# Kernel optimization log

Hardware: AMD Instinct MI355X
Metric: run time of the kernel (lower is better)

Reference implementation:

```python
import jax, jax.numpy as jnp
import numpy as np

B, L, D, H = 8, 512, 512, 8
E, G = 4, 2            # primary experts, ghost experts
THRESH = 0.01          # ghost_activation_threshold
EPS = 1e-5             # LayerNorm eps (torch default)


def _ln(x, s, b):
    m = x.mean(-1, keepdims=True)
    v = ((x - m) ** 2).mean(-1, keepdims=True)
    return (x - m) * jax.lax.rsqrt(v + EPS) * s + b


def _expert(x, ln1_s, ln1_b, wqkv, bqkv, wo, bo, ln2_s, ln2_b, w1, b1, w2, b2):
    # Pre-norm transformer block: MHA + residual, FFN + residual (dropout=0)
    Bn, Ln, Dn = x.shape
    dh = Dn // H
    xn = _ln(x, ln1_s, ln1_b)
    qkv = xn @ wqkv + bqkv                      # [B,L,3D]
    q, k, v = jnp.split(qkv, 3, axis=-1)
    heads = lambda t: t.reshape(Bn, Ln, H, dh).transpose(0, 2, 1, 3)
    q, k, v = heads(q), heads(k), heads(v)      # [B,H,L,dh]
    scores = jnp.einsum('bhqd,bhkd->bhqk', q, k) / np.sqrt(dh).astype(np.float32)
    attn = jax.nn.softmax(scores, axis=-1)
    o = jnp.einsum('bhqk,bhkd->bhqd', attn, v).transpose(0, 2, 1, 3).reshape(Bn, Ln, Dn)
    x = x + o @ wo + bo
    h = _ln(x, ln2_s, ln2_b)
    x = x + jax.nn.gelu(h @ w1 + b1) @ w2 + b2
    return x


def _make_params(key, n, d):
    ks = jax.random.split(key, 4)
    s = 0.02
    return dict(
        ln1_s=jnp.ones((n, d)), ln1_b=jnp.zeros((n, d)),
        wqkv=jax.random.normal(ks[0], (n, d, 3 * d)) * s, bqkv=jnp.zeros((n, 3 * d)),
        wo=jax.random.normal(ks[1], (n, d, d)) * s, bo=jnp.zeros((n, d)),
        ln2_s=jnp.ones((n, d)), ln2_b=jnp.zeros((n, d)),
        w1=jax.random.normal(ks[2], (n, d, 4 * d)) * s, b1=jnp.zeros((n, 4 * d)),
        w2=jax.random.normal(ks[3], (n, 4 * d, d)) * s, b2=jnp.zeros((n, d)))


def setup_inputs() -> dict:
    key = jax.random.key(0)
    k1, k2, k3 = jax.random.split(key, 3)
    inp = {'x': jax.random.normal(k1, (B, L, D), jnp.float32), 'step': 100}
    for pre, n, k in (('p_', E, k2), ('g_', G, k3)):
        for name, arr in _make_params(k, n, D).items():
            inp[pre + name] = arr
    return inp


def reference(x, step,
              p_ln1_s, p_ln1_b, p_wqkv, p_bqkv, p_wo, p_bo, p_ln2_s, p_ln2_b, p_w1, p_b1, p_w2, p_b2,
              g_ln1_s, g_ln1_b, g_wqkv, g_bqkv, g_wo, g_bo, g_ln2_s, g_ln2_b, g_w1, g_b1, g_w2, g_b2):
    pp = (p_ln1_s, p_ln1_b, p_wqkv, p_bqkv, p_wo, p_bo, p_ln2_s, p_ln2_b, p_w1, p_b1, p_w2, p_b2)
    gp = (g_ln1_s, g_ln1_b, g_wqkv, g_bqkv, g_wo, g_bo, g_ln2_s, g_ln2_b, g_w1, g_b1, g_w2, g_b2)
    run = jax.vmap(lambda ps: _expert(x, *ps))
    prim = run(pp)                               # [E,B,L,D]
    # --- saturation metrics (statistics only; detached like .item() in torch) ---
    mean_eo = prim.mean(axis=(1, 2))             # [E,D]
    nrm = mean_eo / jnp.linalg.norm(mean_eo, axis=1, keepdims=True)
    gram = nrm @ nrm.T                           # [E,E]
    ortho = 1.0 - jnp.mean((gram - jnp.eye(E, dtype=gram.dtype)) ** 2)
    recon = prim.mean(axis=0)                    # [B,L,D]
    uvar = jnp.var(x - recon, ddof=1)            # torch.var unbiased default
    sat = jax.lax.stop_gradient(ortho * uvar)
    # --- ghost activation (initial state: all dormant -> ghost 0 gets 0.01) ---
    base = jnp.zeros((G,), x.dtype).at[0].set(0.01)
    rates = jnp.where(sat > THRESH, base, jnp.zeros((G,), x.dtype))
    ghost = jax.vmap(lambda ps: _expert(x, *ps))(gp) * rates[:, None, None, None]  # [G,B,L,D]
    # combine: mean over all (primary + ghost) expert outputs
    out = jnp.concatenate([prim, ghost], axis=0).mean(axis=0)  # [B,L,D]
    return out
```

## Files before the change

### kernel.cpp

```cpp
#include <hip/hip_runtime.h>

typedef __bf16 bf16;
typedef __bf16 bf16x8 __attribute__((ext_vector_type(8)));
typedef float  f32x4  __attribute__((ext_vector_type(4)));

#define AS1 __attribute__((address_space(1)))
#define AS3 __attribute__((address_space(3)))

__device__ __forceinline__ void async16(const void* g, void* l) {
  __builtin_amdgcn_global_load_lds((const AS1 unsigned int*)g, (AS3 unsigned int*)l, 16, 0, 0);
}

__device__ __forceinline__ float gelu_tanh(float u) {
  return 0.5f * u * (1.f + tanhf(0.7978845608028654f * (u + 0.044715f * u * u * u)));
}

__global__ __launch_bounds__(256) void transpose_cvt(const float* pbase, const float* gbase,
                                                     bf16* dst, int K, int M) {
  __shared__ float tile[32][33];
  const int z = blockIdx.z;
  const float* src = (z < 4) ? pbase + (size_t)z * K * M : gbase;
  bf16* d = dst + (size_t)z * M * K;
  const int mBlk = blockIdx.x * 32, kBlk = blockIdx.y * 32;
  for (int i = 0; i < 4; i++)
    tile[threadIdx.y + i * 8][threadIdx.x] =
        src[(size_t)(kBlk + threadIdx.y + i * 8) * M + mBlk + threadIdx.x];
  __syncthreads();
  for (int i = 0; i < 4; i++)
    d[(size_t)(mBlk + threadIdx.y + i * 8) * K + kBlk + threadIdx.x] =
        (bf16)tile[threadIdx.x][threadIdx.y + i * 8];
}

__global__ __launch_bounds__(256) void ln_kernel(const float* in, long long inStrideZ,
                                                 const float* sP, const float* bP,
                                                 const float* sG, const float* bG, bf16* out) {
  const int t = blockIdx.x, z = blockIdx.y, tid = threadIdx.x;
  const float* xr = in + (size_t)z * inStrideZ + (size_t)t * 512;
  float v0 = xr[tid], v1 = xr[tid + 256];
  float s1 = v0 + v1, s2 = v0 * v0 + v1 * v1;
  for (int off = 32; off > 0; off >>= 1) { s1 += __shfl_down(s1, off); s2 += __shfl_down(s2, off); }
  __shared__ float red[8];
  __shared__ float mv[2];
  const int wv = tid >> 6, ln = tid & 63;
  if (ln == 0) { red[wv] = s1; red[4 + wv] = s2; }
  __syncthreads();
  if (tid == 0) {
    float a = red[0] + red[1] + red[2] + red[3];
    float b = red[4] + red[5] + red[6] + red[7];
    float mean = a * (1.f / 512.f);
    float var = b * (1.f / 512.f) - mean * mean;
    mv[0] = mean; mv[1] = 1.f / sqrtf(var + 1e-5f);
  }
  __syncthreads();
  const float mean = mv[0], rs = mv[1];
  const float* sc = (z < 4) ? sP + (size_t)z * 512 : sG;
  const float* bi = (z < 4) ? bP + (size_t)z * 512 : bG;
  bf16* orow = out + (size_t)z * 4096 * 512 + (size_t)t * 512;
  orow[tid]       = (bf16)((v0 - mean) * rs * sc[tid] + bi[tid]);
  orow[tid + 256] = (bf16)((v1 - mean) * rs * sc[tid + 256] + bi[tid + 256]);
}

template <int MODE>
__global__ __launch_bounds__(256, 2) void gemm_bt(
    const bf16* Abase, const bf16* Wt, const float* biasP, const float* biasG,
    int K, int M, void* out, const float* resid, long long residStrideZ,
    float* prim_sum, float* mean_acc, float* ghost_out) {
  const int bx = blockIdx.x, by = blockIdx.y, z = blockIdx.z;
  const bf16* A = Abase + (size_t)z * 4096 * K;
  const bf16* B = Wt + (size_t)z * M * K;
  const float* bias = (z < 4) ? biasP + (size_t)z * M : biasG;
  __shared__ bf16 As[128 * 64];
  __shared__ bf16 Bs[128 * 64];
  const int tid = threadIdx.x, wave = tid >> 6, l = tid & 63;
  const int m16 = l & 15, q4 = l >> 4;
  const int wm = wave & 1, wn = wave >> 1;
  f32x4 zero4 = {0.f, 0.f, 0.f, 0.f};
  f32x4 acc[4][4];
  for (int i = 0; i < 4; i++) for (int j = 0; j < 4; j++) acc[i][j] = zero4;
  const int rowA0 = by * 128, rowB0 = bx * 128;

  for (int kt = 0; kt < K; kt += 64) {
    __syncthreads();
    for (int i = 0; i < 4; i++) {
      int s = i * 256 + tid, r = s >> 3, kb = s & 7;
      int col = kt + ((kb ^ (r & 7)) << 3);
      async16(A + (size_t)(rowA0 + r) * K + col, &As[(i * 256 + wave * 64) * 8]);
      async16(B + (size_t)(rowB0 + r) * K + col, &Bs[(i * 256 + wave * 64) * 8]);
    }
    __syncthreads();
    for (int ks = 0; ks < 2; ks++) {
      bf16x8 af[4], bfr[4];
      for (int mi = 0; mi < 4; mi++) {
        int r = wm * 64 + mi * 16 + m16, kb = ks * 4 + q4;
        af[mi] = *(const bf16x8*)&As[r * 64 + ((kb ^ (r & 7)) << 3)];
      }
      for (int ni = 0; ni < 4; ni++) {
        int r = wn * 64 + ni * 16 + m16, kb = ks * 4 + q4;
        bfr[ni] = *(const bf16x8*)&Bs[r * 64 + ((kb ^ (r & 7)) << 3)];
      }
      for (int mi = 0; mi < 4; mi++)
        for (int ni = 0; ni < 4; ni++)
          acc[mi][ni] = __builtin_amdgcn_mfma_f32_16x16x32_bf16(af[mi], bfr[ni], acc[mi][ni], 0, 0, 0);
    }
  }

  const int col0 = rowB0 + wn * 64, row0 = rowA0 + wm * 64;
  if constexpr (MODE == 3) {
    for (int ni = 0; ni < 4; ni++) {
      int col = col0 + ni * 16 + m16;
      float bb = bias[col];
      float csum = 0.f;
      for (int mi = 0; mi < 4; mi++) {
        for (int cr = 0; cr < 4; cr++) {
          int row = row0 + mi * 16 + q4 * 4 + cr;
          float v = acc[mi][ni][cr] + bb +
                    resid[(size_t)z * residStrideZ + (size_t)row * 512 + col];
          if (z < 4) { atomicAdd(&prim_sum[(size_t)row * 512 + col], v); csum += v; }
          else ghost_out[(size_t)row * 512 + col] = v;
        }
      }
      if (z < 4) {
        csum += __shfl_xor(csum, 16);
        csum += __shfl_xor(csum, 32);
        if (q4 == 0) atomicAdd(&mean_acc[z * 512 + col], csum);
      }
    }
  } else {
    for (int ni = 0; ni < 4; ni++) {
      int col = col0 + ni * 16 + m16;
      float bb = bias[col];
      for (int mi = 0; mi < 4; mi++) {
        for (int cr = 0; cr < 4; cr++) {
          int row = row0 + mi * 16 + q4 * 4 + cr;
          float v = acc[mi][ni][cr] + bb;
          if constexpr (MODE == 0) {
            ((bf16*)out)[(size_t)z * 4096 * M + (size_t)row * M + col] = (bf16)v;
          } else if constexpr (MODE == 1) {
            v += resid[(size_t)row * 512 + col];
            ((float*)out)[(size_t)z * 4096 * 512 + (size_t)row * 512 + col] = v;
          } else {
            ((bf16*)out)[(size_t)z * 4096 * M + (size_t)row * M + col] = (bf16)gelu_tanh(v);
          }
        }
      }
    }
  }
}

__global__ __launch_bounds__(256, 2) void attn_kernel(const bf16* qkv, bf16* o) {
  const int qt = blockIdx.x, bh = blockIdx.y, z = blockIdx.z;
  const int b = bh >> 3, h = bh & 7;
  const bf16* base = qkv + (size_t)z * 4096 * 1536 + (size_t)b * 512 * 1536;
  __shared__ bf16 Qs[128 * 64];
  __shared__ bf16 Ks[64 * 64];
  __shared__ bf16 Vt[64 * 72];
  __shared__ bf16 Ps[4][32 * 72];
  const int tid = threadIdx.x, wave = tid >> 6, l = tid & 63;
  const int m16 = l & 15, q4 = l >> 4;
  f32x4 zero4 = {0.f, 0.f, 0.f, 0.f};

  for (int i = 0; i < 4; i++) {
    int s = i * 256 + tid, r = s >> 3, kb = s & 7;
    async16(base + (size_t)(qt * 128 + r) * 1536 + h * 64 + ((kb ^ (r & 7)) << 3),
            &Qs[(i * 256 + wave * 64) * 8]);
  }
  f32x4 Oacc[2][4];
  float m_run[2][4], l_run[2][4];
  for (int rt = 0; rt < 2; rt++)
    for (int cr = 0; cr < 4; cr++) { m_run[rt][cr] = -3.0e38f; l_run[rt][cr] = 0.f; }
  for (int rt = 0; rt < 2; rt++) for (int dt = 0; dt < 4; dt++) Oacc[rt][dt] = zero4;
  __syncthreads();
  bf16x8 qf[2][2];
  for (int rt = 0; rt < 2; rt++)
    for (int ks = 0; ks < 2; ks++) {
      int r = wave * 32 + rt * 16 + m16, kb = ks * 4 + q4;
      qf[rt][ks] = *(const bf16x8*)&Qs[r * 64 + ((kb ^ (r & 7)) << 3)];
    }

  for (int kt = 0; kt < 8; kt++) {
    __syncthreads();
    for (int i = 0; i < 2; i++) {
      int s = i * 256 + tid, r = s >> 3, kb = s & 7;
      async16(base + (size_t)(kt * 64 + r) * 1536 + 512 + h * 64 + ((kb ^ (r & 7)) << 3),
              &Ks[(i * 256 + wave * 64) * 8]);
    }
    {
      int d = tid & 63, kbase = (tid >> 6) * 2;
      for (int i = 0; i < 8; i++) {
        int k0 = kbase + i * 8;
        bf16 a0 = base[(size_t)(kt * 64 + k0) * 1536 + 1024 + h * 64 + d];
        bf16 a1 = base[(size_t)(kt * 64 + k0 + 1) * 1536 + 1024 + h * 64 + d];
        Vt[d * 72 + k0] = a0; Vt[d * 72 + k0 + 1] = a1;
      }
    }
    __syncthreads();
    f32x4 S[2][4];
    for (int rt = 0; rt < 2; rt++)
      for (int ct = 0; ct < 4; ct++) {
        f32x4 a = zero4;
        for (int ks = 0; ks < 2; ks++) {
          int n = ct * 16 + m16, kb = ks * 4 + q4;
          bf16x8 kf = *(const bf16x8*)&Ks[n * 64 + ((kb ^ (n & 7)) << 3)];
          a = __builtin_amdgcn_mfma_f32_16x16x32_bf16(qf[rt][ks], kf, a, 0, 0, 0);
        }
        S[rt][ct] = a * 0.125f;
      }
    float alpha[2][4];
    for (int rt = 0; rt < 2; rt++)
      for (int cr = 0; cr < 4; cr++) {
        float mx = fmaxf(fmaxf(S[rt][0][cr], S[rt][1][cr]), fmaxf(S[rt][2][cr], S[rt][3][cr]));
        mx = fmaxf(mx, __shfl_xor(mx, 1)); mx = fmaxf(mx, __shfl_xor(mx, 2));
        mx = fmaxf(mx, __shfl_xor(mx, 4)); mx = fmaxf(mx, __shfl_xor(mx, 8));
        float mnew = fmaxf(m_run[rt][cr], mx);
        float al = __expf(m_run[rt][cr] - mnew);
        m_run[rt][cr] = mnew;
        float rs = 0.f;
        for (int ct = 0; ct < 4; ct++) {
          float p = __expf(S[rt][ct][cr] - mnew);
          S[rt][ct][cr] = p; rs += p;
        }
        rs += __shfl_xor(rs, 1); rs += __shfl_xor(rs, 2);
        rs += __shfl_xor(rs, 4); rs += __shfl_xor(rs, 8);
        l_run[rt][cr] = l_run[rt][cr] * al + rs;
        alpha[rt][cr] = al;
      }
    for (int rt = 0; rt < 2; rt++)
      for (int dt = 0; dt < 4; dt++)
        for (int cr = 0; cr < 4; cr++) Oacc[rt][dt][cr] *= alpha[rt][cr];
    bf16* pw = &Ps[wave][0];
    for (int rt = 0; rt < 2; rt++)
      for (int ct = 0; ct < 4; ct++)
        for (int cr = 0; cr < 4; cr++)
          pw[(rt * 16 + q4 * 4 + cr) * 72 + ct * 16 + m16] = (bf16)S[rt][ct][cr];
    for (int rt = 0; rt < 2; rt++)
      for (int dt = 0; dt < 4; dt++) {
        f32x4 a = Oacc[rt][dt];
        for (int ks = 0; ks < 2; ks++) {
          bf16x8 pf = *(const bf16x8*)&pw[(rt * 16 + m16) * 72 + ks * 32 + q4 * 8];
          bf16x8 vf = *(const bf16x8*)&Vt[(dt * 16 + m16) * 72 + ks * 32 + q4 * 8];
          a = __builtin_amdgcn_mfma_f32_16x16x32_bf16(pf, vf, a, 0, 0, 0);
        }
        Oacc[rt][dt] = a;
      }
  }
  bf16* ob = o + (size_t)z * 4096 * 512 + (size_t)(b * 512 + qt * 128 + wave * 32) * 512 + h * 64;
  for (int rt = 0; rt < 2; rt++)
    for (int dt = 0; dt < 4; dt++)
      for (int cr = 0; cr < 4; cr++) {
        int r = rt * 16 + q4 * 4 + cr;
        ob[(size_t)r * 512 + dt * 16 + m16] = (bf16)(Oacc[rt][dt][cr] / l_run[rt][cr]);
      }
}

__global__ __launch_bounds__(256) void stats_diff(const float* x, const float* ps, float* accum) {
  const int tid0 = blockIdx.x * blockDim.x + threadIdx.x;
  float s = 0.f, s2 = 0.f;
  const f32x4* xv = (const f32x4*)x;
  const f32x4* pv = (const f32x4*)ps;
  for (int it = 0; it < 2; it++) {
    int i = tid0 + it * 262144;
    f32x4 d = xv[i] - pv[i] * 0.25f;
    s += d[0] + d[1] + d[2] + d[3];
    s2 += d[0] * d[0] + d[1] * d[1] + d[2] * d[2] + d[3] * d[3];
  }
  for (int off = 32; off > 0; off >>= 1) { s += __shfl_down(s, off); s2 += __shfl_down(s2, off); }
  __shared__ float r1[4], r2[4];
  if ((threadIdx.x & 63) == 0) { r1[threadIdx.x >> 6] = s; r2[threadIdx.x >> 6] = s2; }
  __syncthreads();
  if (threadIdx.x == 0) {
    atomicAdd(&accum[0], r1[0] + r1[1] + r1[2] + r1[3]);
    atomicAdd(&accum[1], r2[0] + r2[1] + r2[2] + r2[3]);
  }
}

__global__ void finalize_k(const float* mean_acc, const float* accum, float* rate) {
  const int l = threadIdx.x;
  float me[4][8];
  for (int e = 0; e < 4; e++)
    for (int j = 0; j < 8; j++) me[e][j] = mean_acc[e * 512 + l * 8 + j] * (1.f / 4096.f);
  float dot[4][4];
  for (int e = 0; e < 4; e++)
    for (int f = e; f < 4; f++) {
      float d = 0.f;
      for (int j = 0; j < 8; j++) d += me[e][j] * me[f][j];
      for (int off = 32; off > 0; off >>= 1) d += __shfl_xor(d, off);
      dot[e][f] = d; dot[f][e] = d;
    }
  float nrm[4];
  for (int e = 0; e < 4; e++) nrm[e] = sqrtf(dot[e][e]);
  float acc = 0.f;
  for (int e = 0; e < 4; e++)
    for (int f = 0; f < 4; f++) {
      float g = dot[e][f] / (nrm[e] * nrm[f]) - (e == f ? 1.f : 0.f);
      acc += g * g;
    }
  float ortho = 1.f - acc * (1.f / 16.f);
  float n = 2097152.f;
  float uvar = (accum[1] - accum[0] * accum[0] / n) / (n - 1.f);
  float sat = ortho * uvar;
  if (l == 0) rate[0] = (sat > 0.01f) ? 0.01f : 0.f;
}

__global__ __launch_bounds__(256) void combine_k(const float* prim, const float* ghost,
                                                 const float* rate, float* out) {
  float r = rate[0];
  int i = blockIdx.x * blockDim.x + threadIdx.x;
  const f32x4* p = (const f32x4*)prim;
  const f32x4* g = (const f32x4*)ghost;
  ((f32x4*)out)[i] = (p[i] + r * g[i]) * (1.f / 6.f);
}

extern "C" void kernel_launch(void* const* d_in, const int* in_sizes, int n_in,
                              void* d_out, int out_size, void* d_ws, size_t ws_size,
                              hipStream_t stream) {
  const float* x       = (const float*)d_in[0];
  const float* p_ln1_s = (const float*)d_in[2];
  const float* p_ln1_b = (const float*)d_in[3];
  const float* p_wqkv  = (const float*)d_in[4];
  const float* p_bqkv  = (const float*)d_in[5];
  const float* p_wo    = (const float*)d_in[6];
  const float* p_bo    = (const float*)d_in[7];
  const float* p_ln2_s = (const float*)d_in[8];
  const float* p_ln2_b = (const float*)d_in[9];
  const float* p_w1    = (const float*)d_in[10];
  const float* p_b1    = (const float*)d_in[11];
  const float* p_w2    = (const float*)d_in[12];
  const float* p_b2    = (const float*)d_in[13];
  const float* g_ln1_s = (const float*)d_in[14];
  const float* g_ln1_b = (const float*)d_in[15];
  const float* g_wqkv  = (const float*)d_in[16];
  const float* g_bqkv  = (const float*)d_in[17];
  const float* g_wo    = (const float*)d_in[18];
  const float* g_bo    = (const float*)d_in[19];
  const float* g_ln2_s = (const float*)d_in[20];
  const float* g_ln2_b = (const float*)d_in[21];
  const float* g_w1    = (const float*)d_in[22];
  const float* g_b1    = (const float*)d_in[23];
  const float* g_w2    = (const float*)d_in[24];
  const float* g_b2    = (const float*)d_in[25];

  char* ws = (char*)d_ws;
  size_t off = 0;
  auto alloc = [&](size_t bytes) { void* p = ws + off; off += (bytes + 255) & ~(size_t)255; return p; };
  bf16* wt_qkv   = (bf16*)alloc(5ull * 1536 * 512 * 2);
  bf16* wt_wo    = (bf16*)alloc(5ull * 512 * 512 * 2);
  bf16* wt_w1    = (bf16*)alloc(5ull * 2048 * 512 * 2);
  bf16* wt_w2    = (bf16*)alloc(5ull * 512 * 2048 * 2);
  bf16* act_a    = (bf16*)alloc(5ull * 4096 * 512 * 2);
  bf16* big      = (bf16*)alloc(5ull * 4096 * 2048 * 2);
  float* x1      = (float*)alloc(5ull * 4096 * 512 * 4);
  float* prim_sum  = (float*)alloc(4096ull * 512 * 4);
  float* ghost_out = (float*)alloc(4096ull * 512 * 4);
  float* mean_acc  = (float*)alloc(4 * 512 * 4);
  float* accum     = (float*)alloc(256);

  hipMemsetAsync(prim_sum, 0, 4096ull * 512 * 4, stream);
  hipMemsetAsync(mean_acc, 0, 4 * 512 * 4, stream);
  hipMemsetAsync(accum, 0, 16, stream);

  dim3 tb(32, 8);
  transpose_cvt<<<dim3(1536 / 32, 512 / 32, 5), tb, 0, stream>>>(p_wqkv, g_wqkv, wt_qkv, 512, 1536);
  transpose_cvt<<<dim3(512 / 32, 512 / 32, 5), tb, 0, stream>>>(p_wo, g_wo, wt_wo, 512, 512);
  transpose_cvt<<<dim3(2048 / 32, 512 / 32, 5), tb, 0, stream>>>(p_w1, g_w1, wt_w1, 512, 2048);
  transpose_cvt<<<dim3(512 / 32, 2048 / 32, 5), tb, 0, stream>>>(p_w2, g_w2, wt_w2, 2048, 512);

  ln_kernel<<<dim3(4096, 5), 256, 0, stream>>>(x, 0, p_ln1_s, p_ln1_b, g_ln1_s, g_ln1_b, act_a);
  gemm_bt<0><<<dim3(12, 32, 5), 256, 0, stream>>>(act_a, wt_qkv, p_bqkv, g_bqkv, 512, 1536,
                                                  big, nullptr, 0, nullptr, nullptr, nullptr);
  attn_kernel<<<dim3(4, 64, 5), 256, 0, stream>>>(big, act_a);
  gemm_bt<1><<<dim3(4, 32, 5), 256, 0, stream>>>(act_a, wt_wo, p_bo, g_bo, 512, 512,
                                                 x1, x, 0, nullptr, nullptr, nullptr);
  ln_kernel<<<dim3(4096, 5), 256, 0, stream>>>(x1, 4096ll * 512, p_ln2_s, p_ln2_b, g_ln2_s, g_ln2_b, act_a);
  gemm_bt<2><<<dim3(16, 32, 5), 256, 0, stream>>>(act_a, wt_w1, p_b1, g_b1, 512, 2048,
                                                  big, nullptr, 0, nullptr, nullptr, nullptr);
  gemm_bt<3><<<dim3(4, 32, 5), 256, 0, stream>>>(big, wt_w2, p_b2, g_b2, 2048, 512,
                                                 nullptr, x1, 4096ll * 512, prim_sum, mean_acc, ghost_out);
  stats_diff<<<dim3(1024), 256, 0, stream>>>(x, prim_sum, accum);
  finalize_k<<<1, 64, 0, stream>>>(mean_acc, accum, accum + 2);
  combine_k<<<dim3(2048), 256, 0, stream>>>(prim_sum, ghost_out, accum + 2, (float*)d_out);
}
```

Baseline: 546.7 us.

## Fold LN1 into QKV weights, store bf16 intermediates, stage GEMM epilogues via LDS

```diff
diff --git a/kernel.cpp b/kernel.cpp
--- a/kernel.cpp
+++ b/kernel.cpp
@@ -11,38 +11,57 @@
   __builtin_amdgcn_global_load_lds((const AS1 unsigned int*)g, (AS3 unsigned int*)l, 16, 0, 0);
 }
 
-__device__ __forceinline__ float gelu_tanh(float u) {
-  return 0.5f * u * (1.f + tanhf(0.7978845608028654f * (u + 0.044715f * u * u * u)));
-}
-
-__global__ __launch_bounds__(256) void transpose_cvt(const float* pbase, const float* gbase,
-                                                     bf16* dst, int K, int M) {
+__device__ __forceinline__ float gelu_fast(float u) {
+  float z = 0.7978845608028654f * (u + 0.044715f * u * u * u);
+  z = fminf(fmaxf(z, -15.f), 15.f);
+  float t = __expf(2.f * z);
+  return u * t / (t + 1.f);
+}
+
+template <int FOLD>
+__global__ __launch_bounds__(256) void transpose_cvt(
+    const float* pbase, const float* gbase, bf16* dst, int K, int M,
+    const float* lnsP, const float* lnbP, const float* lnsG, const float* lnbG,
+    const float* b0P, const float* b0G, float* bias_eff) {
   __shared__ float tile[32][33];
   const int z = blockIdx.z;
   const float* src = (z < 4) ? pbase + (size_t)z * K * M : gbase;
   bf16* d = dst + (size_t)z * M * K;
   const int mBlk = blockIdx.x * 32, kBlk = blockIdx.y * 32;
+  const int tx = threadIdx.x, ty = threadIdx.y;
   for (int i = 0; i < 4; i++)
-    tile[threadIdx.y + i * 8][threadIdx.x] =
-        src[(size_t)(kBlk + threadIdx.y + i * 8) * M + mBlk + threadIdx.x];
-  __syncthreads();
-  for (int i = 0; i < 4; i++)
-    d[(size_t)(mBlk + threadIdx.y + i * 8) * K + kBlk + threadIdx.x] =
-        (bf16)tile[threadIdx.x][threadIdx.y + i * 8];
-}
-
-__global__ __launch_bounds__(256) void ln_kernel(const float* in, long long inStrideZ,
-                                                 const float* sP, const float* bP,
-                                                 const float* sG, const float* bG, bf16* out) {
-  const int t = blockIdx.x, z = blockIdx.y, tid = threadIdx.x;
-  const float* xr = in + (size_t)z * inStrideZ + (size_t)t * 512;
+    tile[ty + i * 8][tx] = src[(size_t)(kBlk + ty + i * 8) * M + mBlk + tx];
+  __syncthreads();
+  if constexpr (FOLD) {
+    const float* s  = (z < 4) ? lnsP + (size_t)z * 512 : lnsG;
+    const float* bb = (z < 4) ? lnbP + (size_t)z * 512 : lnbG;
+    const float sk = s[kBlk + tx];
+    for (int i = 0; i < 4; i++)
+      d[(size_t)(mBlk + ty + i * 8) * K + kBlk + tx] = (bf16)(tile[tx][ty + i * 8] * sk);
+    if (ty == 0) {
+      float acc = 0.f;
+      for (int kk = 0; kk < 32; kk++) acc += bb[kBlk + kk] * tile[kk][tx];
+      if (kBlk == 0) {
+        const float* b0 = (z < 4) ? b0P + (size_t)z * M : b0G;
+        acc += b0[mBlk + tx];
+      }
+      atomicAdd(&bias_eff[(size_t)z * M + mBlk + tx], acc);
+    }
+  } else {
+    for (int i = 0; i < 4; i++)
+      d[(size_t)(mBlk + ty + i * 8) * K + kBlk + tx] = (bf16)tile[tx][ty + i * 8];
+  }
+}
+
+__global__ __launch_bounds__(256) void ln_plain(const float* x, bf16* out) {
+  const int t = blockIdx.x, tid = threadIdx.x;
+  const float* xr = x + (size_t)t * 512;
   float v0 = xr[tid], v1 = xr[tid + 256];
   float s1 = v0 + v1, s2 = v0 * v0 + v1 * v1;
   for (int off = 32; off > 0; off >>= 1) { s1 += __shfl_down(s1, off); s2 += __shfl_down(s2, off); }
   __shared__ float red[8];
   __shared__ float mv[2];
-  const int wv = tid >> 6, ln = tid & 63;
-  if (ln == 0) { red[wv] = s1; red[4 + wv] = s2; }
+  if ((tid & 63) == 0) { red[tid >> 6] = s1; red[4 + (tid >> 6)] = s2; }
   __syncthreads();
   if (tid == 0) {
     float a = red[0] + red[1] + red[2] + red[3];
@@ -53,24 +72,50 @@
   }
   __syncthreads();
   const float mean = mv[0], rs = mv[1];
+  bf16* o = out + (size_t)t * 512;
+  o[tid]       = (bf16)((v0 - mean) * rs);
+  o[tid + 256] = (bf16)((v1 - mean) * rs);
+}
+
+__global__ __launch_bounds__(256) void ln2_kernel(const bf16* in, const float* sP, const float* bP,
+                                                  const float* sG, const float* bG, bf16* out) {
+  const int t = blockIdx.x, z = blockIdx.y, tid = threadIdx.x;
+  const bf16* xr = in + (size_t)z * 4096 * 512 + (size_t)t * 512;
+  float v0 = (float)xr[tid], v1 = (float)xr[tid + 256];
+  float s1 = v0 + v1, s2 = v0 * v0 + v1 * v1;
+  for (int off = 32; off > 0; off >>= 1) { s1 += __shfl_down(s1, off); s2 += __shfl_down(s2, off); }
+  __shared__ float red[8];
+  __shared__ float mv[2];
+  if ((tid & 63) == 0) { red[tid >> 6] = s1; red[4 + (tid >> 6)] = s2; }
+  __syncthreads();
+  if (tid == 0) {
+    float a = red[0] + red[1] + red[2] + red[3];
+    float b = red[4] + red[5] + red[6] + red[7];
+    float mean = a * (1.f / 512.f);
+    float var = b * (1.f / 512.f) - mean * mean;
+    mv[0] = mean; mv[1] = 1.f / sqrtf(var + 1e-5f);
+  }
+  __syncthreads();
+  const float mean = mv[0], rs = mv[1];
   const float* sc = (z < 4) ? sP + (size_t)z * 512 : sG;
   const float* bi = (z < 4) ? bP + (size_t)z * 512 : bG;
-  bf16* orow = out + (size_t)z * 4096 * 512 + (size_t)t * 512;
-  orow[tid]       = (bf16)((v0 - mean) * rs * sc[tid] + bi[tid]);
-  orow[tid + 256] = (bf16)((v1 - mean) * rs * sc[tid + 256] + bi[tid + 256]);
+  bf16* o = out + (size_t)z * 4096 * 512 + (size_t)t * 512;
+  o[tid]       = (bf16)((v0 - mean) * rs * sc[tid] + bi[tid]);
+  o[tid + 256] = (bf16)((v1 - mean) * rs * sc[tid + 256] + bi[tid + 256]);
 }
 
 template <int MODE>
 __global__ __launch_bounds__(256, 2) void gemm_bt(
-    const bf16* Abase, const bf16* Wt, const float* biasP, const float* biasG,
-    int K, int M, void* out, const float* resid, long long residStrideZ,
-    float* prim_sum, float* mean_acc, float* ghost_out) {
+    const bf16* Abase, long long aStrideZ, const bf16* Wt,
+    const float* biasP, const float* biasG, int K, int M,
+    bf16* out, const void* resid, long long residStrideZ) {
   const int bx = blockIdx.x, by = blockIdx.y, z = blockIdx.z;
-  const bf16* A = Abase + (size_t)z * 4096 * K;
+  const bf16* A = Abase + (size_t)z * aStrideZ;
   const bf16* B = Wt + (size_t)z * M * K;
   const float* bias = (z < 4) ? biasP + (size_t)z * M : biasG;
-  __shared__ bf16 As[128 * 64];
-  __shared__ bf16 Bs[128 * 64];
+  __shared__ bf16 smem[128 * 136];
+  bf16* As = smem;
+  bf16* Bs = smem + 128 * 64;
   const int tid = threadIdx.x, wave = tid >> 6, l = tid & 63;
   const int m16 = l & 15, q4 = l >> 4;
   const int wm = wave & 1, wn = wave >> 1;
@@ -104,46 +149,32 @@
     }
   }
 
-  const int col0 = rowB0 + wn * 64, row0 = rowA0 + wm * 64;
-  if constexpr (MODE == 3) {
-    for (int ni = 0; ni < 4; ni++) {
-      int col = col0 + ni * 16 + m16;
-      float bb = bias[col];
-      float csum = 0.f;
-      for (int mi = 0; mi < 4; mi++) {
-        for (int cr = 0; cr < 4; cr++) {
-          int row = row0 + mi * 16 + q4 * 4 + cr;
-          float v = acc[mi][ni][cr] + bb +
-                    resid[(size_t)z * residStrideZ + (size_t)row * 512 + col];
-          if (z < 4) { atomicAdd(&prim_sum[(size_t)row * 512 + col], v); csum += v; }
-          else ghost_out[(size_t)row * 512 + col] = v;
-        }
-      }
-      if (z < 4) {
-        csum += __shfl_xor(csum, 16);
-        csum += __shfl_xor(csum, 32);
-        if (q4 == 0) atomicAdd(&mean_acc[z * 512 + col], csum);
-      }
-    }
-  } else {
-    for (int ni = 0; ni < 4; ni++) {
-      int col = col0 + ni * 16 + m16;
-      float bb = bias[col];
-      for (int mi = 0; mi < 4; mi++) {
-        for (int cr = 0; cr < 4; cr++) {
-          int row = row0 + mi * 16 + q4 * 4 + cr;
-          float v = acc[mi][ni][cr] + bb;
-          if constexpr (MODE == 0) {
-            ((bf16*)out)[(size_t)z * 4096 * M + (size_t)row * M + col] = (bf16)v;
-          } else if constexpr (MODE == 1) {
-            v += resid[(size_t)row * 512 + col];
-            ((float*)out)[(size_t)z * 4096 * 512 + (size_t)row * 512 + col] = v;
-          } else {
-            ((bf16*)out)[(size_t)z * 4096 * M + (size_t)row * M + col] = (bf16)gelu_tanh(v);
-          }
-        }
-      }
-    }
+  __syncthreads();
+  for (int ni = 0; ni < 4; ni++) {
+    int coll = wn * 64 + ni * 16 + m16;
+    float bb = bias[rowB0 + coll];
+    for (int mi = 0; mi < 4; mi++) {
+      for (int cr = 0; cr < 4; cr++) {
+        float v = acc[mi][ni][cr] + bb;
+        if constexpr (MODE == 2) v = gelu_fast(v);
+        smem[(wm * 64 + mi * 16 + q4 * 4 + cr) * 136 + coll] = (bf16)v;
+      }
+    }
+  }
+  __syncthreads();
+  bf16* ob = out + (size_t)z * 4096 * M;
+  for (int p = 0; p < 8; p++) {
+    int r = p * 16 + (tid >> 4), c0 = (tid & 15) * 8;
+    bf16x8 vv = *(const bf16x8*)&smem[r * 136 + c0];
+    if constexpr (MODE == 1) {
+      const float* rx = (const float*)resid + (size_t)(rowA0 + r) * 512 + rowB0 + c0;
+      for (int j = 0; j < 8; j++) vv[j] = (bf16)((float)vv[j] + rx[j]);
+    } else if constexpr (MODE == 3) {
+      const bf16* rx = (const bf16*)resid + (size_t)z * residStrideZ + (size_t)(rowA0 + r) * 512 + rowB0 + c0;
+      bf16x8 rv = *(const bf16x8*)rx;
+      for (int j = 0; j < 8; j++) vv[j] = (bf16)((float)vv[j] + (float)rv[j]);
+    }
+    *(bf16x8*)&ob[(size_t)(rowA0 + r) * M + rowB0 + c0] = vv;
   }
 }
 
@@ -184,14 +215,10 @@
       async16(base + (size_t)(kt * 64 + r) * 1536 + 512 + h * 64 + ((kb ^ (r & 7)) << 3),
               &Ks[(i * 256 + wave * 64) * 8]);
     }
-    {
-      int d = tid & 63, kbase = (tid >> 6) * 2;
-      for (int i = 0; i < 8; i++) {
-        int k0 = kbase + i * 8;
-        bf16 a0 = base[(size_t)(kt * 64 + k0) * 1536 + 1024 + h * 64 + d];
-        bf16 a1 = base[(size_t)(kt * 64 + k0 + 1) * 1536 + 1024 + h * 64 + d];
-        Vt[d * 72 + k0] = a0; Vt[d * 72 + k0 + 1] = a1;
-      }
+    for (int p = 0; p < 2; p++) {
+      int k = p * 32 + (tid >> 3), d0 = (tid & 7) * 8;
+      bf16x8 v8 = *(const bf16x8*)&base[(size_t)(kt * 64 + k) * 1536 + 1024 + h * 64 + d0];
+      for (int j = 0; j < 8; j++) Vt[(d0 + j) * 72 + k] = v8[j];
     }
     __syncthreads();
     f32x4 S[2][4];
@@ -252,22 +279,37 @@
       }
 }
 
-__global__ __launch_bounds__(256) void stats_diff(const float* x, const float* ps, float* accum) {
-  const int tid0 = blockIdx.x * blockDim.x + threadIdx.x;
-  float s = 0.f, s2 = 0.f;
-  const f32x4* xv = (const f32x4*)x;
-  const f32x4* pv = (const f32x4*)ps;
-  for (int it = 0; it < 2; it++) {
-    int i = tid0 + it * 262144;
-    f32x4 d = xv[i] - pv[i] * 0.25f;
-    s += d[0] + d[1] + d[2] + d[3];
-    s2 += d[0] * d[0] + d[1] * d[1] + d[2] * d[2] + d[3] * d[3];
-  }
-  for (int off = 32; off > 0; off >>= 1) { s += __shfl_down(s, off); s2 += __shfl_down(s2, off); }
+__global__ __launch_bounds__(256) void stats_k(const bf16* eout, const float* x,
+                                               float* prim_sum, float* mean_acc, float* accum) {
+  const int r0 = blockIdx.x * 32;
+  const int tid = threadIdx.x;
+  const int c0 = tid * 2;
+  float cs[4][2] = {{0.f,0.f},{0.f,0.f},{0.f,0.f},{0.f,0.f}};
+  float sd = 0.f, sd2 = 0.f;
+  for (int rr = 0; rr < 32; rr++) {
+    int row = r0 + rr;
+    float s0 = 0.f, s1 = 0.f;
+    for (int e = 0; e < 4; e++) {
+      const bf16* p = &eout[((size_t)e * 4096 + row) * 512 + c0];
+      float f0 = (float)p[0], f1 = (float)p[1];
+      cs[e][0] += f0; cs[e][1] += f1;
+      s0 += f0; s1 += f1;
+    }
+    prim_sum[(size_t)row * 512 + c0]     = s0;
+    prim_sum[(size_t)row * 512 + c0 + 1] = s1;
+    float d0 = x[(size_t)row * 512 + c0]     - s0 * 0.25f;
+    float d1 = x[(size_t)row * 512 + c0 + 1] - s1 * 0.25f;
+    sd += d0 + d1; sd2 += d0 * d0 + d1 * d1;
+  }
+  for (int e = 0; e < 4; e++) {
+    atomicAdd(&mean_acc[e * 512 + c0],     cs[e][0]);
+    atomicAdd(&mean_acc[e * 512 + c0 + 1], cs[e][1]);
+  }
+  for (int off = 32; off > 0; off >>= 1) { sd += __shfl_down(sd, off); sd2 += __shfl_down(sd2, off); }
   __shared__ float r1[4], r2[4];
-  if ((threadIdx.x & 63) == 0) { r1[threadIdx.x >> 6] = s; r2[threadIdx.x >> 6] = s2; }
-  __syncthreads();
-  if (threadIdx.x == 0) {
+  if ((tid & 63) == 0) { r1[tid >> 6] = sd; r2[tid >> 6] = sd2; }
+  __syncthreads();
+  if (tid == 0) {
     atomicAdd(&accum[0], r1[0] + r1[1] + r1[2] + r1[3]);
     atomicAdd(&accum[1], r2[0] + r2[1] + r2[2] + r2[3]);
   }
@@ -301,13 +343,15 @@
   if (l == 0) rate[0] = (sat > 0.01f) ? 0.01f : 0.f;
 }
 
-__global__ __launch_bounds__(256) void combine_k(const float* prim, const float* ghost,
+__global__ __launch_bounds__(256) void combine_k(const float* prim, const bf16* ghost,
                                                  const float* rate, float* out) {
   float r = rate[0];
-  int i = blockIdx.x * blockDim.x + threadIdx.x;
-  const f32x4* p = (const f32x4*)prim;
-  const f32x4* g = (const f32x4*)ghost;
-  ((f32x4*)out)[i] = (p[i] + r * g[i]) * (1.f / 6.f);
+  int i = blockIdx.x * 256 + threadIdx.x;
+  f32x4 p = ((const f32x4*)prim)[i];
+  const bf16* g = ghost + (size_t)i * 4;
+  f32x4 o;
+  for (int j = 0; j < 4; j++) o[j] = (p[j] + r * (float)g[j]) * (1.f / 6.f);
+  ((f32x4*)out)[i] = o;
 }
 
 extern "C" void kernel_launch(void* const* d_in, const int* in_sizes, int n_in,
@@ -346,36 +390,42 @@
   bf16* wt_wo    = (bf16*)alloc(5ull * 512 * 512 * 2);
   bf16* wt_w1    = (bf16*)alloc(5ull * 2048 * 512 * 2);
   bf16* wt_w2    = (bf16*)alloc(5ull * 512 * 2048 * 2);
+  bf16* xn       = (bf16*)alloc(4096ull * 512 * 2);
   bf16* act_a    = (bf16*)alloc(5ull * 4096 * 512 * 2);
   bf16* big      = (bf16*)alloc(5ull * 4096 * 2048 * 2);
-  float* x1      = (float*)alloc(5ull * 4096 * 512 * 4);
-  float* prim_sum  = (float*)alloc(4096ull * 512 * 4);
-  float* ghost_out = (float*)alloc(4096ull * 512 * 4);
-  float* mean_acc  = (float*)alloc(4 * 512 * 4);
-  float* accum     = (float*)alloc(256);
-
-  hipMemsetAsync(prim_sum, 0, 4096ull * 512 * 4, stream);
+  bf16* x1       = (bf16*)alloc(5ull * 4096 * 512 * 2);
+  bf16* eout     = (bf16*)alloc(5ull * 4096 * 512 * 2);
+  float* prim_sum = (float*)alloc(4096ull * 512 * 4);
+  float* bias_eff = (float*)alloc(5ull * 1536 * 4);
+  float* mean_acc = (float*)alloc(4 * 512 * 4);
+  float* accum    = (float*)alloc(256);
+
+  hipMemsetAsync(bias_eff, 0, 5ull * 1536 * 4, stream);
   hipMemsetAsync(mean_acc, 0, 4 * 512 * 4, stream);
   hipMemsetAsync(accum, 0, 16, stream);
 
   dim3 tb(32, 8);
-  transpose_cvt<<<dim3(1536 / 32, 512 / 32, 5), tb, 0, stream>>>(p_wqkv, g_wqkv, wt_qkv, 512, 1536);
-  transpose_cvt<<<dim3(512 / 32, 512 / 32, 5), tb, 0, stream>>>(p_wo, g_wo, wt_wo, 512, 512);
-  transpose_cvt<<<dim3(2048 / 32, 512 / 32, 5), tb, 0, stream>>>(p_w1, g_w1, wt_w1, 512, 2048);
-  transpose_cvt<<<dim3(512 / 32, 2048 / 32, 5), tb, 0, stream>>>(p_w2, g_w2, wt_w2, 2048, 512);
-
-  ln_kernel<<<dim3(4096, 5), 256, 0, stream>>>(x, 0, p_ln1_s, p_ln1_b, g_ln1_s, g_ln1_b, act_a);
-  gemm_bt<0><<<dim3(12, 32, 5), 256, 0, stream>>>(act_a, wt_qkv, p_bqkv, g_bqkv, 512, 1536,
-                                                  big, nullptr, 0, nullptr, nullptr, nullptr);
+  transpose_cvt<1><<<dim3(48, 16, 5), tb, 0, stream>>>(p_wqkv, g_wqkv, wt_qkv, 512, 1536,
+      p_ln1_s, p_ln1_b, g_ln1_s, g_ln1_b, p_bqkv, g_bqkv, bias_eff);
+  transpose_cvt<0><<<dim3(16, 16, 5), tb, 0, stream>>>(p_wo, g_wo, wt_wo, 512, 512,
+      nullptr, nullptr, nullptr, nullptr, nullptr, nullptr, nullptr);
+  transpose_cvt<0><<<dim3(64, 16, 5), tb, 0, stream>>>(p_w1, g_w1, wt_w1, 512, 2048,
+      nullptr, nullptr, nullptr, nullptr, nullptr, nullptr, nullptr);
+  transpose_cvt<0><<<dim3(16, 64, 5), tb, 0, stream>>>(p_w2, g_w2, wt_w2, 2048, 512,
+      nullptr, nullptr, nullptr, nullptr, nullptr, nullptr, nullptr);
+
+  ln_plain<<<dim3(4096), 256, 0, stream>>>(x, xn);
+  gemm_bt<0><<<dim3(12, 32, 5), 256, 0, stream>>>(xn, 0, wt_qkv, bias_eff, bias_eff + 4ull * 1536,
+                                                  512, 1536, big, nullptr, 0);
   attn_kernel<<<dim3(4, 64, 5), 256, 0, stream>>>(big, act_a);
-  gemm_bt<1><<<dim3(4, 32, 5), 256, 0, stream>>>(act_a, wt_wo, p_bo, g_bo, 512, 512,
-                                                 x1, x, 0, nullptr, nullptr, nullptr);
-  ln_kernel<<<dim3(4096, 5), 256, 0, stream>>>(x1, 4096ll * 512, p_ln2_s, p_ln2_b, g_ln2_s, g_ln2_b, act_a);
-  gemm_bt<2><<<dim3(16, 32, 5), 256, 0, stream>>>(act_a, wt_w1, p_b1, g_b1, 512, 2048,
-                                                  big, nullptr, 0, nullptr, nullptr, nullptr);
-  gemm_bt<3><<<dim3(4, 32, 5), 256, 0, stream>>>(big, wt_w2, p_b2, g_b2, 2048, 512,
-                                                 nullptr, x1, 4096ll * 512, prim_sum, mean_acc, ghost_out);
-  stats_diff<<<dim3(1024), 256, 0, stream>>>(x, prim_sum, accum);
+  gemm_bt<1><<<dim3(4, 32, 5), 256, 0, stream>>>(act_a, 4096ll * 512, wt_wo, p_bo, g_bo,
+                                                 512, 512, x1, x, 0);
+  ln2_kernel<<<dim3(4096, 5), 256, 0, stream>>>(x1, p_ln2_s, p_ln2_b, g_ln2_s, g_ln2_b, act_a);
+  gemm_bt<2><<<dim3(16, 32, 5), 256, 0, stream>>>(act_a, 4096ll * 512, wt_w1, p_b1, g_b1,
+                                                  512, 2048, big, nullptr, 0);
+  gemm_bt<3><<<dim3(4, 32, 5), 256, 0, stream>>>(big, 4096ll * 2048, wt_w2, p_b2, g_b2,
+                                                 2048, 512, eout, x1, 4096ll * 512);
+  stats_k<<<dim3(128), 256, 0, stream>>>(eout, x, prim_sum, mean_acc, accum);
   finalize_k<<<1, 64, 0, stream>>>(mean_acc, accum, accum + 2);
-  combine_k<<<dim3(2048), 256, 0, stream>>>(prim_sum, ghost_out, accum + 2, (float*)d_out);
-}
+  combine_k<<<dim3(2048), 256, 0, stream>>>(prim_sum, eout + 4ull * 4096 * 512, accum + 2, (float*)d_out);
+}
```

After: 509.5 us. -6.8%, faster.
